# Kernel optimization log

Hardware: AMD Instinct MI355X
Metric: run time of the kernel (lower is better)

The kernel has to match this reference:

```python
import jax, jax.numpy as jnp
import numpy as np

N_NODES = 100000
N_EDGES = 1600000
D = 64


def setup_inputs() -> dict:
    key = jax.random.key(0)
    k1, k2, k3, k4 = jax.random.split(key, 4)
    graph_embedding = jax.random.normal(k1, (N_NODES, D), dtype=jnp.float32)
    # xavier_uniform_ on a (1, D) tensor: bound = sqrt(6 / (1 + D))
    bound = float(np.sqrt(6.0 / (1 + D)))
    weight = jax.random.uniform(k2, (1, D), dtype=jnp.float32, minval=-bound, maxval=bound)
    src = jax.random.randint(k3, (N_EDGES,), 0, N_NODES, dtype=jnp.int32)
    dst = jax.random.randint(k4, (N_EDGES,), 0, N_NODES, dtype=jnp.int32)
    return {"graph_embedding": graph_embedding, "weight": weight, "src": src, "dst": dst}


def reference(graph_embedding, weight, src, dst):
    # emb = elu(x * w) per node, then copy_u/sum over edges:
    # out[d] = sum over edges (s -> d) of emb[s]
    emb = jax.nn.elu(graph_embedding * weight)          # [N, D]
    msgs = emb[src]                                     # [E, D] gathered source messages
    out = jax.ops.segment_sum(msgs, dst, num_segments=graph_embedding.shape[0])
    return out
```

## Files before the change

### kernel.cpp

```cpp
#include <hip/hip_runtime.h>

#define D 64
#define D4 (D / 4)
#define SBSHIFT 9
#define SBROWS 512
#define CHUNK_E 8192
#define STAGE_CAP 8704
#define NCH_MAX 256
#define NSB_MAX 256

typedef float f32x4 __attribute__((ext_vector_type(4)));

__device__ __forceinline__ float elu1(float z) {
    return z > 0.0f ? z : expm1f(z);
}

__device__ __forceinline__ unsigned int bfpair(float a, float b) {
    unsigned int ua = __float_as_uint(a);
    unsigned int ub = __float_as_uint(b);
    ua = (ua + 0x7FFFu + ((ua >> 16) & 1u)) >> 16;
    ub = (ub + 0x7FFFu + ((ub >> 16) & 1u)) & 0xFFFF0000u;
    return ub | ua;
}

__global__ void emb_kernel(const float* __restrict__ x,
                           const float* __restrict__ w,
                           uint4* __restrict__ emb16,
                           int total8) {
    int i = blockIdx.x * blockDim.x + threadIdx.x;
    if (i >= total8) return;
    f32x4 a = __builtin_nontemporal_load((const f32x4*)x + 2 * i);
    f32x4 b = __builtin_nontemporal_load((const f32x4*)x + 2 * i + 1);
    float4 wa = ((const float4*)w)[(2 * i) & 15];
    float4 wb = ((const float4*)w)[(2 * i + 1) & 15];
    uint4 o;
    o.x = bfpair(elu1(a.x * wa.x), elu1(a.y * wa.y));
    o.y = bfpair(elu1(a.z * wa.z), elu1(a.w * wa.w));
    o.z = bfpair(elu1(b.x * wb.x), elu1(b.y * wb.y));
    o.w = bfpair(elu1(b.z * wb.z), elu1(b.w * wb.w));
    emb16[i] = o;
}

__global__ __launch_bounds__(512) void chunk_sort_kernel(
        const int* __restrict__ src, const int* __restrict__ dst,
        int* __restrict__ slots_lin,
        int* __restrict__ cbase,
        int n_edges) {
    __shared__ int hist[256], base[256], cur[256];
    __shared__ int wsum[4];
    __shared__ int stage[CHUNK_E];
    const int tid = threadIdx.x;
    const int lane = tid & 63, wid = tid >> 6;
    const int c0  = blockIdx.x * CHUNK_E;
    const int kn  = min(CHUNK_E, n_edges - c0);
    const int kn4 = kn >> 2;
    const int tail = kn & 3;

    if (tid < 256) hist[tid] = 0;
    __syncthreads();
    const int4* dst4 = (const int4*)(dst + c0);
    for (int k = tid; k < kn4; k += 512) {
        int4 dv = dst4[k];
        atomicAdd(&hist[dv.x >> SBSHIFT], 1);
        atomicAdd(&hist[dv.y >> SBSHIFT], 1);
        atomicAdd(&hist[dv.z >> SBSHIFT], 1);
        atomicAdd(&hist[dv.w >> SBSHIFT], 1);
    }
    if (tid < tail)
        atomicAdd(&hist[dst[c0 + (kn4 << 2) + tid] >> SBSHIFT], 1);
    __syncthreads();
    int h = 0, incl = 0;
    if (tid < 256) {
        h = hist[tid];
        incl = h;
        #pragma unroll
        for (int off = 1; off < 64; off <<= 1) {
            int t = __shfl_up(incl, off, 64);
            if (lane >= off) incl += t;
        }
        if (lane == 63) wsum[wid] = incl;
    }
    __syncthreads();
    if (tid < 256) {
        int pre = 0;
        for (int k = 0; k < wid; k++) pre += wsum[k];
        int e = pre + incl - h;
        base[tid] = e;
        cur[tid]  = e;
    }
    __syncthreads();
    const int4* src4 = (const int4*)(src + c0);
    for (int k = tid; k < kn4; k += 512) {
        int4 dv = dst4[k];
        int4 sv = src4[k];
        int pos;
        pos = atomicAdd(&cur[dv.x >> SBSHIFT], 1);
        stage[pos] = ((dv.x & (SBROWS - 1)) << 17) | sv.x;
        pos = atomicAdd(&cur[dv.y >> SBSHIFT], 1);
        stage[pos] = ((dv.y & (SBROWS - 1)) << 17) | sv.y;
        pos = atomicAdd(&cur[dv.z >> SBSHIFT], 1);
        stage[pos] = ((dv.z & (SBROWS - 1)) << 17) | sv.z;
        pos = atomicAdd(&cur[dv.w >> SBSHIFT], 1);
        stage[pos] = ((dv.w & (SBROWS - 1)) << 17) | sv.w;
    }
    if (tid < tail) {
        int k = (kn4 << 2) + tid;
        int d = dst[c0 + k], s = src[c0 + k];
        int pos = atomicAdd(&cur[d >> SBSHIFT], 1);
        stage[pos] = ((d & (SBROWS - 1)) << 17) | s;
    }
    __syncthreads();
    for (int j = tid; j < kn; j += 512)
        slots_lin[c0 + j] = stage[j];
    if (tid < 256) cbase[blockIdx.x * 257 + tid] = base[tid];
    if (tid == 0)  cbase[blockIdx.x * 257 + 256] = kn;
}

__global__ void sbtot_kernel(const int* __restrict__ cbase,
                             int* __restrict__ sbtot, int NSB, int NCH) {
    __shared__ int wsum[4];
    const int s = blockIdx.x;
    const int tid = threadIdx.x;
    int v = 0;
    if (tid < NCH)
        v = cbase[tid * 257 + s + 1] - cbase[tid * 257 + s];
    #pragma unroll
    for (int off = 1; off < 64; off <<= 1) v += __shfl_xor(v, off, 64);
    if ((tid & 63) == 0) wsum[tid >> 6] = v;
    __syncthreads();
    if (tid == 0) sbtot[s] = wsum[0] + wsum[1] + wsum[2] + wsum[3];
}

__global__ void sb_scan2_kernel(const int* __restrict__ sbtot,
                                int* __restrict__ sb_base,
                                int* __restrict__ node_off,
                                int NSB, int n_nodes) {
    __shared__ int wsum[4];
    const int tid = threadIdx.x;
    int v = (tid < NSB) ? sbtot[tid] : 0;
    int incl = v;
    #pragma unroll
    for (int off = 1; off < 64; off <<= 1) {
        int t = __shfl_up(incl, off, 64);
        if ((tid & 63) >= off) incl += t;
    }
    if ((tid & 63) == 63) wsum[tid >> 6] = incl;
    __syncthreads();
    int pre = 0;
    for (int k = 0; k < (tid >> 6); k++) pre += wsum[k];
    if (tid < NSB) sb_base[tid] = pre + incl - v;
    if (tid == 0) {
        int g = wsum[0] + wsum[1] + wsum[2] + wsum[3];
        sb_base[NSB] = g;
        node_off[n_nodes] = g;
    }
}

__global__ __launch_bounds__(512) void fine_sort_kernel(
        const int* __restrict__ slots_lin,
        const int* __restrict__ cbase,
        const int* __restrict__ sb_base,
        int* __restrict__ sorted2,
        int* __restrict__ node_off,
        int n_nodes, int NCH) {
    __shared__ int rstart[NCH_MAX], rc[NCH_MAX];
    __shared__ int counts[SBROWS], cur[SBROWS];
    __shared__ int wsum[8];
    __shared__ int stage_out[STAGE_CAP];
    const int s = blockIdx.x;
    const int tid = threadIdx.x;
    const int wid = tid >> 6, lane = tid & 63;

    if (tid < NCH) {
        int a = cbase[tid * 257 + s];
        int b = cbase[tid * 257 + s + 1];
        rstart[tid] = tid * CHUNK_E + a;
        rc[tid] = b - a;
    }
    counts[tid] = 0;
    __syncthreads();
    const int sbb = sb_base[s];
    const int T   = sb_base[s + 1] - sbb;
    const bool fast = (T <= STAGE_CAP);
    for (int c = wid; c < NCH; c += 8) {
        int n = rc[c], st = rstart[c];
        for (int j = lane; j < n; j += 64)
            atomicAdd(&counts[((unsigned)slots_lin[st + j]) >> 17], 1);
    }
    __syncthreads();
    int v = counts[tid];
    int incl = v;
    #pragma unroll
    for (int off = 1; off < 64; off <<= 1) {
        int t = __shfl_up(incl, off, 64);
        if (lane >= off) incl += t;
    }
    if (lane == 63) wsum[wid] = incl;
    __syncthreads();
    int pre = 0;
    for (int k = 0; k < wid; k++) pre += wsum[k];
    int e0 = pre + incl - v;
    cur[tid] = fast ? e0 : sbb + e0;
    int g0 = (s << SBSHIFT) + tid;
    if (g0 < n_nodes) node_off[g0] = sbb + e0;
    __syncthreads();
    for (int c = wid; c < NCH; c += 8) {
        int n = rc[c], st = rstart[c];
        for (int j = lane; j < n; j += 64) {
            int pl = slots_lin[st + j];
            int r = ((unsigned)pl) >> 17;
            int pos = atomicAdd(&cur[r], 1);
            if (fast) stage_out[pos] = pl & 0x1FFFF;
            else      sorted2[pos]   = pl & 0x1FFFF;
        }
    }
    __syncthreads();
    if (fast) {
        for (int i = tid; i < T; i += 512)
            sorted2[sbb + i] = stage_out[i];
    }
}

__global__ void gather_sum_kernel(const unsigned int* __restrict__ emb16,
                                  const int* __restrict__ sorted2,
                                  const int* __restrict__ node_off,
                                  float* __restrict__ out, int n_nodes) {
    int wave = (blockIdx.x * blockDim.x + threadIdx.x) >> 6;
    if (wave >= n_nodes) return;
    const int lane = threadIdx.x & 63;
    const int g = lane >> 3;
    const int c = lane & 7;
    const int beg = node_off[wave], end = node_off[wave + 1];
    const int4* row = (const int4*)emb16;

    float acc[8] = {0.f, 0.f, 0.f, 0.f, 0.f, 0.f, 0.f, 0.f};
    int e = beg + g;
    for (; e + 8 < end; e += 16) {
        int s0 = __builtin_nontemporal_load(sorted2 + e);
        int s1 = __builtin_nontemporal_load(sorted2 + e + 8);
        int4 u0 = row[s0 * 8 + c];
        int4 u1 = row[s1 * 8 + c];
        acc[0] += __uint_as_float((unsigned)u0.x << 16) + __uint_as_float((unsigned)u1.x << 16);
        acc[1] += __uint_as_float(u0.x & 0xFFFF0000u)   + __uint_as_float(u1.x & 0xFFFF0000u);
        acc[2] += __uint_as_float((unsigned)u0.y << 16) + __uint_as_float((unsigned)u1.y << 16);
        acc[3] += __uint_as_float(u0.y & 0xFFFF0000u)   + __uint_as_float(u1.y & 0xFFFF0000u);
        acc[4] += __uint_as_float((unsigned)u0.z << 16) + __uint_as_float((unsigned)u1.z << 16);
        acc[5] += __uint_as_float(u0.z & 0xFFFF0000u)   + __uint_as_float(u1.z & 0xFFFF0000u);
        acc[6] += __uint_as_float((unsigned)u0.w << 16) + __uint_as_float((unsigned)u1.w << 16);
        acc[7] += __uint_as_float(u0.w & 0xFFFF0000u)   + __uint_as_float(u1.w & 0xFFFF0000u);
    }
    if (e < end) {
        int s0 = __builtin_nontemporal_load(sorted2 + e);
        int4 u0 = row[s0 * 8 + c];
        acc[0] += __uint_as_float((unsigned)u0.x << 16);
        acc[1] += __uint_as_float(u0.x & 0xFFFF0000u);
        acc[2] += __uint_as_float((unsigned)u0.y << 16);
        acc[3] += __uint_as_float(u0.y & 0xFFFF0000u);
        acc[4] += __uint_as_float((unsigned)u0.z << 16);
        acc[5] += __uint_as_float(u0.z & 0xFFFF0000u);
        acc[6] += __uint_as_float((unsigned)u0.w << 16);
        acc[7] += __uint_as_float(u0.w & 0xFFFF0000u);
    }
    #pragma unroll
    for (int off = 8; off <= 32; off <<= 1) {
        #pragma unroll
        for (int k = 0; k < 8; k++) acc[k] += __shfl_xor(acc[k], off, 64);
    }
    if (g == 0) {
        f32x4* out4 = (f32x4*)out;
        f32x4 o0 = {acc[0], acc[1], acc[2], acc[3]};
        f32x4 o1 = {acc[4], acc[5], acc[6], acc[7]};
        __builtin_nontemporal_store(o0, out4 + wave * D4 + c * 2);
        __builtin_nontemporal_store(o1, out4 + wave * D4 + c * 2 + 1);
    }
}

__global__ void zero_out_kernel(float* __restrict__ out, int total4) {
    int i = blockIdx.x * blockDim.x + threadIdx.x;
    if (i < total4) ((float4*)out)[i] = make_float4(0.f, 0.f, 0.f, 0.f);
}

__global__ void scatter_fused_kernel(const float* __restrict__ x,
                                     const float* __restrict__ w,
                                     const int* __restrict__ src,
                                     const int* __restrict__ dst,
                                     float* __restrict__ out, int n_edges) {
    int t = blockIdx.x * blockDim.x + threadIdx.x;
    int e = t >> 4;
    int c = t & 15;
    if (e >= n_edges) return;
    int s = src[e];
    int d = dst[e];
    float4 xv = ((const float4*)x)[s * D4 + c];
    float4 wv = ((const float4*)w)[c];
    float* o = out + d * D + c * 4;
    unsafeAtomicAdd(o + 0, elu1(xv.x * wv.x));
    unsafeAtomicAdd(o + 1, elu1(xv.y * wv.y));
    unsafeAtomicAdd(o + 2, elu1(xv.z * wv.z));
    unsafeAtomicAdd(o + 3, elu1(xv.w * wv.w));
}

extern "C" void kernel_launch(void* const* d_in, const int* in_sizes, int n_in,
                              void* d_out, int out_size, void* d_ws, size_t ws_size,
                              hipStream_t stream) {
    const float* x   = (const float*)d_in[0];
    const float* w   = (const float*)d_in[1];
    const int*   src = (const int*)d_in[2];
    const int*   dst = (const int*)d_in[3];
    float* out = (float*)d_out;

    const int n_nodes = in_sizes[0] / D;
    const int n_edges = in_sizes[2];
    const int total4  = n_nodes * D4;
    const int total8  = n_nodes * 8;
    const int block = 256;

    const int NSB = (n_nodes + SBROWS - 1) >> SBSHIFT;
    const int NCH = (n_edges + CHUNK_E - 1) / CHUNK_E;

    auto align16 = [](size_t v) { return (v + 15) & ~size_t(15); };
    const size_t emb_b      = align16((size_t)n_nodes * D * 2);
    const size_t slots_b    = align16((size_t)NCH * CHUNK_E * 4);
    const size_t cbase_b    = align16((size_t)NCH * 257 * 4);
    const size_t sbtot_b    = align16((size_t)NSB * 4);
    const size_t sbbase_b   = align16((size_t)(NSB + 1) * 4);
    const size_t sorted2_b  = align16((size_t)n_edges * 4);
    const size_t nodeoff_b  = align16((size_t)(n_nodes + 1) * 4);
    const size_t need = emb_b + slots_b + cbase_b + sbtot_b + sbbase_b +
                        sorted2_b + nodeoff_b;

    if (ws_size >= need && n_nodes <= 131072 && NSB <= NSB_MAX && NCH <= NCH_MAX) {
        char* p = (char*)d_ws;
        unsigned int* emb16 = (unsigned int*)p;  p += emb_b;
        int* slots_lin = (int*)p;  p += slots_b;
        int* cbase     = (int*)p;  p += cbase_b;
        int* sbtot     = (int*)p;  p += sbtot_b;
        int* sb_base   = (int*)p;  p += sbbase_b;
        int* sorted2   = (int*)p;  p += sorted2_b;
        int* node_off  = (int*)p;

        emb_kernel<<<(total8 + block - 1) / block, block, 0, stream>>>(
            x, w, (uint4*)emb16, total8);
        chunk_sort_kernel<<<NCH, 512, 0, stream>>>(
            src, dst, slots_lin, cbase, n_edges);
        sbtot_kernel<<<NSB, 256, 0, stream>>>(cbase, sbtot, NSB, NCH);
        sb_scan2_kernel<<<1, 256, 0, stream>>>(sbtot, sb_base, node_off,
                                               NSB, n_nodes);
        fine_sort_kernel<<<NSB, 512, 0, stream>>>(
            slots_lin, cbase, sb_base, sorted2, node_off, n_nodes, NCH);
        const int wave_blocks = (n_nodes * 64 + block - 1) / block;
        gather_sum_kernel<<<wave_blocks, block, 0, stream>>>(
            emb16, sorted2, node_off, out, n_nodes);
    } else {
        zero_out_kernel<<<(total4 + block - 1) / block, block, 0, stream>>>(out, total4);
        const int nt = n_edges * 16;
        scatter_fused_kernel<<<(nt + block - 1) / block, block, 0, stream>>>(
            x, w, src, dst, out, n_edges);
    }
}
```

Before: 161.8 us.

## Fuse fine sort and gather-sum into per-half-superblock kernel with LDS staging

Replaces the superblock-total, scan, fine-sort and gather-sum kernels with one kernel that runs two blocks per superblock. Each block counts and buckets its 256 destination rows in shared memory, then gathers bf16 source rows and writes the sums directly. This removes the global sorted-index and node-offset round trips and three kernel launches. In exchange each superblock's slot list is read by two blocks with half the entries filtered out, there are only about 400 blocks, and an atomic fallback path covers overflowing buckets.

```diff
diff --git a/kernel.cpp b/kernel.cpp
--- a/kernel.cpp
+++ b/kernel.cpp
@@ -4,8 +4,9 @@
 #define D4 (D / 4)
 #define SBSHIFT 9
 #define SBROWS 512
+#define HALF 256
 #define CHUNK_E 8192
-#define STAGE_CAP 8704
+#define STAGE_CAP 4608
 #define NCH_MAX 256
 #define NSB_MAX 256
 
@@ -116,162 +117,140 @@
     if (tid == 0)  cbase[blockIdx.x * 257 + 256] = kn;
 }
 
-__global__ void sbtot_kernel(const int* __restrict__ cbase,
-                             int* __restrict__ sbtot, int NSB, int NCH) {
-    __shared__ int wsum[4];
-    const int s = blockIdx.x;
-    const int tid = threadIdx.x;
-    int v = 0;
-    if (tid < NCH)
-        v = cbase[tid * 257 + s + 1] - cbase[tid * 257 + s];
-    #pragma unroll
-    for (int off = 1; off < 64; off <<= 1) v += __shfl_xor(v, off, 64);
-    if ((tid & 63) == 0) wsum[tid >> 6] = v;
-    __syncthreads();
-    if (tid == 0) sbtot[s] = wsum[0] + wsum[1] + wsum[2] + wsum[3];
-}
-
-__global__ void sb_scan2_kernel(const int* __restrict__ sbtot,
-                                int* __restrict__ sb_base,
-                                int* __restrict__ node_off,
-                                int NSB, int n_nodes) {
-    __shared__ int wsum[4];
-    const int tid = threadIdx.x;
-    int v = (tid < NSB) ? sbtot[tid] : 0;
-    int incl = v;
-    #pragma unroll
-    for (int off = 1; off < 64; off <<= 1) {
-        int t = __shfl_up(incl, off, 64);
-        if ((tid & 63) >= off) incl += t;
-    }
-    if ((tid & 63) == 63) wsum[tid >> 6] = incl;
-    __syncthreads();
-    int pre = 0;
-    for (int k = 0; k < (tid >> 6); k++) pre += wsum[k];
-    if (tid < NSB) sb_base[tid] = pre + incl - v;
-    if (tid == 0) {
-        int g = wsum[0] + wsum[1] + wsum[2] + wsum[3];
-        sb_base[NSB] = g;
-        node_off[n_nodes] = g;
-    }
-}
-
-__global__ __launch_bounds__(512) void fine_sort_kernel(
+__global__ __launch_bounds__(512) void sb_gather_kernel(
+        const unsigned int* __restrict__ emb16,
         const int* __restrict__ slots_lin,
         const int* __restrict__ cbase,
-        const int* __restrict__ sb_base,
-        int* __restrict__ sorted2,
-        int* __restrict__ node_off,
-        int n_nodes, int NCH) {
+        float* __restrict__ out, int n_nodes, int NCH) {
     __shared__ int rstart[NCH_MAX], rc[NCH_MAX];
-    __shared__ int counts[SBROWS], cur[SBROWS];
-    __shared__ int wsum[8];
-    __shared__ int stage_out[STAGE_CAP];
-    const int s = blockIdx.x;
-    const int tid = threadIdx.x;
+    __shared__ int counts[HALF], cur[HALF];
+    __shared__ int wsum[4];
+    __shared__ int stage[STAGE_CAP];
+    const int sb   = blockIdx.x >> 1;
+    const int half = blockIdx.x & 1;
+    const int tid  = threadIdx.x;
     const int wid = tid >> 6, lane = tid & 63;
+    const int rbase = half << 8;
+    const int lo = (sb << SBSHIFT) + rbase;
+    const int rows_here = min(HALF, n_nodes - lo);
+    if (rows_here <= 0) return;
 
     if (tid < NCH) {
-        int a = cbase[tid * 257 + s];
-        int b = cbase[tid * 257 + s + 1];
+        int a = cbase[tid * 257 + sb];
+        int b = cbase[tid * 257 + sb + 1];
         rstart[tid] = tid * CHUNK_E + a;
         rc[tid] = b - a;
     }
-    counts[tid] = 0;
-    __syncthreads();
-    const int sbb = sb_base[s];
-    const int T   = sb_base[s + 1] - sbb;
-    const bool fast = (T <= STAGE_CAP);
-    for (int c = wid; c < NCH; c += 8) {
-        int n = rc[c], st = rstart[c];
-        for (int j = lane; j < n; j += 64)
-            atomicAdd(&counts[((unsigned)slots_lin[st + j]) >> 17], 1);
-    }
-    __syncthreads();
-    int v = counts[tid];
-    int incl = v;
-    #pragma unroll
-    for (int off = 1; off < 64; off <<= 1) {
-        int t = __shfl_up(incl, off, 64);
-        if (lane >= off) incl += t;
-    }
-    if (lane == 63) wsum[wid] = incl;
-    __syncthreads();
-    int pre = 0;
-    for (int k = 0; k < wid; k++) pre += wsum[k];
-    int e0 = pre + incl - v;
-    cur[tid] = fast ? e0 : sbb + e0;
-    int g0 = (s << SBSHIFT) + tid;
-    if (g0 < n_nodes) node_off[g0] = sbb + e0;
+    if (tid < HALF) counts[tid] = 0;
     __syncthreads();
     for (int c = wid; c < NCH; c += 8) {
         int n = rc[c], st = rstart[c];
         for (int j = lane; j < n; j += 64) {
-            int pl = slots_lin[st + j];
-            int r = ((unsigned)pl) >> 17;
-            int pos = atomicAdd(&cur[r], 1);
-            if (fast) stage_out[pos] = pl & 0x1FFFF;
-            else      sorted2[pos]   = pl & 0x1FFFF;
-        }
-    }
-    __syncthreads();
-    if (fast) {
-        for (int i = tid; i < T; i += 512)
-            sorted2[sbb + i] = stage_out[i];
-    }
-}
-
-__global__ void gather_sum_kernel(const unsigned int* __restrict__ emb16,
-                                  const int* __restrict__ sorted2,
-                                  const int* __restrict__ node_off,
-                                  float* __restrict__ out, int n_nodes) {
-    int wave = (blockIdx.x * blockDim.x + threadIdx.x) >> 6;
-    if (wave >= n_nodes) return;
-    const int lane = threadIdx.x & 63;
-    const int g = lane >> 3;
-    const int c = lane & 7;
-    const int beg = node_off[wave], end = node_off[wave + 1];
-    const int4* row = (const int4*)emb16;
-
-    float acc[8] = {0.f, 0.f, 0.f, 0.f, 0.f, 0.f, 0.f, 0.f};
-    int e = beg + g;
-    for (; e + 8 < end; e += 16) {
-        int s0 = __builtin_nontemporal_load(sorted2 + e);
-        int s1 = __builtin_nontemporal_load(sorted2 + e + 8);
-        int4 u0 = row[s0 * 8 + c];
-        int4 u1 = row[s1 * 8 + c];
-        acc[0] += __uint_as_float((unsigned)u0.x << 16) + __uint_as_float((unsigned)u1.x << 16);
-        acc[1] += __uint_as_float(u0.x & 0xFFFF0000u)   + __uint_as_float(u1.x & 0xFFFF0000u);
-        acc[2] += __uint_as_float((unsigned)u0.y << 16) + __uint_as_float((unsigned)u1.y << 16);
-        acc[3] += __uint_as_float(u0.y & 0xFFFF0000u)   + __uint_as_float(u1.y & 0xFFFF0000u);
-        acc[4] += __uint_as_float((unsigned)u0.z << 16) + __uint_as_float((unsigned)u1.z << 16);
-        acc[5] += __uint_as_float(u0.z & 0xFFFF0000u)   + __uint_as_float(u1.z & 0xFFFF0000u);
-        acc[6] += __uint_as_float((unsigned)u0.w << 16) + __uint_as_float((unsigned)u1.w << 16);
-        acc[7] += __uint_as_float(u0.w & 0xFFFF0000u)   + __uint_as_float(u1.w & 0xFFFF0000u);
-    }
-    if (e < end) {
-        int s0 = __builtin_nontemporal_load(sorted2 + e);
-        int4 u0 = row[s0 * 8 + c];
-        acc[0] += __uint_as_float((unsigned)u0.x << 16);
-        acc[1] += __uint_as_float(u0.x & 0xFFFF0000u);
-        acc[2] += __uint_as_float((unsigned)u0.y << 16);
-        acc[3] += __uint_as_float(u0.y & 0xFFFF0000u);
-        acc[4] += __uint_as_float((unsigned)u0.z << 16);
-        acc[5] += __uint_as_float(u0.z & 0xFFFF0000u);
-        acc[6] += __uint_as_float((unsigned)u0.w << 16);
-        acc[7] += __uint_as_float(u0.w & 0xFFFF0000u);
-    }
-    #pragma unroll
-    for (int off = 8; off <= 32; off <<= 1) {
+            int r = (int)(((unsigned)slots_lin[st + j]) >> 17) - rbase;
+            if ((unsigned)r < HALF) atomicAdd(&counts[r], 1);
+        }
+    }
+    __syncthreads();
+    int v = 0, incl = 0;
+    if (tid < HALF) {
+        v = counts[tid];
+        incl = v;
         #pragma unroll
-        for (int k = 0; k < 8; k++) acc[k] += __shfl_xor(acc[k], off, 64);
-    }
-    if (g == 0) {
-        f32x4* out4 = (f32x4*)out;
-        f32x4 o0 = {acc[0], acc[1], acc[2], acc[3]};
-        f32x4 o1 = {acc[4], acc[5], acc[6], acc[7]};
-        __builtin_nontemporal_store(o0, out4 + wave * D4 + c * 2);
-        __builtin_nontemporal_store(o1, out4 + wave * D4 + c * 2 + 1);
+        for (int off = 1; off < 64; off <<= 1) {
+            int t = __shfl_up(incl, off, 64);
+            if (lane >= off) incl += t;
+        }
+        if (lane == 63) wsum[wid] = incl;
+    }
+    __syncthreads();
+    const int T = wsum[0] + wsum[1] + wsum[2] + wsum[3];
+    if (tid < HALF) {
+        int pre = 0;
+        for (int k = 0; k < wid; k++) pre += wsum[k];
+        cur[tid] = pre + incl - v;
+    }
+    __syncthreads();
+    if (T <= STAGE_CAP) {
+        for (int c = wid; c < NCH; c += 8) {
+            int n = rc[c], st = rstart[c];
+            for (int j = lane; j < n; j += 64) {
+                int pl = slots_lin[st + j];
+                int r = (int)(((unsigned)pl) >> 17) - rbase;
+                if ((unsigned)r < HALF) {
+                    int pos = atomicAdd(&cur[r], 1);
+                    stage[pos] = pl & 0x1FFFF;
+                }
+            }
+        }
+        __syncthreads();
+        const int g = lane >> 3, c8 = lane & 7;
+        const int4* row = (const int4*)emb16;
+        for (int r = wid; r < rows_here; r += 8) {
+            const int end_ = cur[r];
+            const int beg_ = end_ - counts[r];
+            float acc[8] = {0.f, 0.f, 0.f, 0.f, 0.f, 0.f, 0.f, 0.f};
+            int e = beg_ + g;
+            for (; e + 8 < end_; e += 16) {
+                int s0 = stage[e];
+                int s1 = stage[e + 8];
+                int4 u0 = row[s0 * 8 + c8];
+                int4 u1 = row[s1 * 8 + c8];
+                acc[0] += __uint_as_float((unsigned)u0.x << 16) + __uint_as_float((unsigned)u1.x << 16);
+                acc[1] += __uint_as_float(u0.x & 0xFFFF0000u)   + __uint_as_float(u1.x & 0xFFFF0000u);
+                acc[2] += __uint_as_float((unsigned)u0.y << 16) + __uint_as_float((unsigned)u1.y << 16);
+                acc[3] += __uint_as_float(u0.y & 0xFFFF0000u)   + __uint_as_float(u1.y & 0xFFFF0000u);
+                acc[4] += __uint_as_float((unsigned)u0.z << 16) + __uint_as_float((unsigned)u1.z << 16);
+                acc[5] += __uint_as_float(u0.z & 0xFFFF0000u)   + __uint_as_float(u1.z & 0xFFFF0000u);
+                acc[6] += __uint_as_float((unsigned)u0.w << 16) + __uint_as_float((unsigned)u1.w << 16);
+                acc[7] += __uint_as_float(u0.w & 0xFFFF0000u)   + __uint_as_float(u1.w & 0xFFFF0000u);
+            }
+            if (e < end_) {
+                int s0 = stage[e];
+                int4 u0 = row[s0 * 8 + c8];
+                acc[0] += __uint_as_float((unsigned)u0.x << 16);
+                acc[1] += __uint_as_float(u0.x & 0xFFFF0000u);
+                acc[2] += __uint_as_float((unsigned)u0.y << 16);
+                acc[3] += __uint_as_float(u0.y & 0xFFFF0000u);
+                acc[4] += __uint_as_float((unsigned)u0.z << 16);
+                acc[5] += __uint_as_float(u0.z & 0xFFFF0000u);
+                acc[6] += __uint_as_float((unsigned)u0.w << 16);
+                acc[7] += __uint_as_float(u0.w & 0xFFFF0000u);
+            }
+            #pragma unroll
+            for (int off = 8; off <= 32; off <<= 1) {
+                #pragma unroll
+                for (int k = 0; k < 8; k++) acc[k] += __shfl_xor(acc[k], off, 64);
+            }
+            if (g == 0) {
+                f32x4* out4 = (f32x4*)out;
+                f32x4 o0 = {acc[0], acc[1], acc[2], acc[3]};
+                f32x4 o1 = {acc[4], acc[5], acc[6], acc[7]};
+                __builtin_nontemporal_store(o0, out4 + (size_t)(lo + r) * D4 + c8 * 2);
+                __builtin_nontemporal_store(o1, out4 + (size_t)(lo + r) * D4 + c8 * 2 + 1);
+            }
+        }
+    } else {
+        float4 z = make_float4(0.f, 0.f, 0.f, 0.f);
+        float4* ob = (float4*)(out + (size_t)lo * D);
+        for (int i = tid; i < rows_here * D4; i += 512) ob[i] = z;
+        __syncthreads();
+        for (int c = wid; c < NCH; c += 8) {
+            int n = rc[c], st = rstart[c];
+            for (int j = lane; j < n; j += 64) {
+                int pl = slots_lin[st + j];
+                int r = (int)(((unsigned)pl) >> 17) - rbase;
+                if ((unsigned)r < HALF) {
+                    int srcid = pl & 0x1FFFF;
+                    float* orow = out + (size_t)(lo + r) * D;
+                    const unsigned* rp = emb16 + (size_t)srcid * 32;
+                    for (int k = 0; k < 32; k++) {
+                        unsigned u = rp[k];
+                        unsafeAtomicAdd(orow + 2 * k,     __uint_as_float(u << 16));
+                        unsafeAtomicAdd(orow + 2 * k + 1, __uint_as_float(u & 0xFFFF0000u));
+                    }
+                }
+            }
+        }
     }
 }
 
@@ -319,38 +298,23 @@
     const int NCH = (n_edges + CHUNK_E - 1) / CHUNK_E;
 
     auto align16 = [](size_t v) { return (v + 15) & ~size_t(15); };
-    const size_t emb_b      = align16((size_t)n_nodes * D * 2);
-    const size_t slots_b    = align16((size_t)NCH * CHUNK_E * 4);
-    const size_t cbase_b    = align16((size_t)NCH * 257 * 4);
-    const size_t sbtot_b    = align16((size_t)NSB * 4);
-    const size_t sbbase_b   = align16((size_t)(NSB + 1) * 4);
-    const size_t sorted2_b  = align16((size_t)n_edges * 4);
-    const size_t nodeoff_b  = align16((size_t)(n_nodes + 1) * 4);
-    const size_t need = emb_b + slots_b + cbase_b + sbtot_b + sbbase_b +
-                        sorted2_b + nodeoff_b;
+    const size_t emb_b   = align16((size_t)n_nodes * D * 2);
+    const size_t slots_b = align16((size_t)NCH * CHUNK_E * 4);
+    const size_t cbase_b = align16((size_t)NCH * 257 * 4);
+    const size_t need = emb_b + slots_b + cbase_b;
 
     if (ws_size >= need && n_nodes <= 131072 && NSB <= NSB_MAX && NCH <= NCH_MAX) {
         char* p = (char*)d_ws;
         unsigned int* emb16 = (unsigned int*)p;  p += emb_b;
         int* slots_lin = (int*)p;  p += slots_b;
-        int* cbase     = (int*)p;  p += cbase_b;
-        int* sbtot     = (int*)p;  p += sbtot_b;
-        int* sb_base   = (int*)p;  p += sbbase_b;
-        int* sorted2   = (int*)p;  p += sorted2_b;
-        int* node_off  = (int*)p;
+        int* cbase     = (int*)p;
 
         emb_kernel<<<(total8 + block - 1) / block, block, 0, stream>>>(
             x, w, (uint4*)emb16, total8);
         chunk_sort_kernel<<<NCH, 512, 0, stream>>>(
             src, dst, slots_lin, cbase, n_edges);
-        sbtot_kernel<<<NSB, 256, 0, stream>>>(cbase, sbtot, NSB, NCH);
-        sb_scan2_kernel<<<1, 256, 0, stream>>>(sbtot, sb_base, node_off,
-                                               NSB, n_nodes);
-        fine_sort_kernel<<<NSB, 512, 0, stream>>>(
-            slots_lin, cbase, sb_base, sorted2, node_off, n_nodes, NCH);
-        const int wave_blocks = (n_nodes * 64 + block - 1) / block;
-        gather_sum_kernel<<<wave_blocks, block, 0, stream>>>(
-            emb16, sorted2, node_off, out, n_nodes);
+        sb_gather_kernel<<<2 * NSB, 512, 0, stream>>>(
+            emb16, slots_lin, cbase, out, n_nodes, NCH);
     } else {
         zero_out_kernel<<<(total4 + block - 1) / block, block, 0, stream>>>(out, total4);
         const int nt = n_edges * 16;
```

After: 165.0 us. 2.0% more time.
